# Kernel tuning notes

Measured on AMD Instinct MI355X. Metric: run time of the kernel, lower is better.

## Reference

```python
import jax, jax.numpy as jnp
import numpy as np

B, H, S_PAST, S_NEW, D = 4, 32, 4096, 16, 128


def setup_inputs() -> dict:
    key = jax.random.key(0)
    k1, k2, k3, k4 = jax.random.split(key, 4)
    return {
        "past_key": jax.random.normal(k1, (B, H, S_PAST, D), dtype=jnp.float32),
        "past_value": jax.random.normal(k2, (B, H, S_PAST, D), dtype=jnp.float32),
        "key_states": jax.random.normal(k3, (B, H, S_NEW, D), dtype=jnp.float32),
        "value_states": jax.random.normal(k4, (B, H, S_NEW, D), dtype=jnp.float32),
    }


def reference(past_key, past_value, key_states, value_states):
    # DynamicCache.update: append new tokens along the sequence axis (dim=-2)
    k = jnp.concatenate([past_key, key_states], axis=-2)   # [B,H,S_past+S_new,D]
    v = jnp.concatenate([past_value, value_states], axis=-2)
    return (k, v)
```

## Files before the change

kernel.cpp:

```cpp
#include <hip/hip_runtime.h>


constexpr unsigned B = 4, H = 32, S_PAST = 4096, S_NEW = 16, D = 128;
constexpr unsigned S_TOT = S_PAST + S_NEW;
constexpr unsigned ROW4  = D / 4;
constexpr unsigned CHUNK4 = S_TOT * ROW4;
constexpr unsigned HALF4 = B * H * CHUNK4;
constexpr unsigned TOTAL4 = 2u * HALF4;

__global__ __launch_bounds__(256) void dyncache_concat_kernel(
    const float4* __restrict__ pk, const float4* __restrict__ pv,
    const float4* __restrict__ nk, const float4* __restrict__ nv,
    float4* __restrict__ out)
{
    const unsigned stride = gridDim.x * blockDim.x;
    for (unsigned i = blockIdx.x * blockDim.x + threadIdx.x; i < TOTAL4; i += stride) {
        unsigned j = i;
        const float4* past = pk;
        const float4* neu  = nk;
        if (j >= HALF4) { j -= HALF4; past = pv; neu = nv; }
        const unsigned bh  = j / CHUNK4;
        const unsigned rem = j - bh * CHUNK4;
        const unsigned s   = rem / ROW4;
        const unsigned d4  = rem - s * ROW4;
        float4 val;
        if (s < S_PAST) {
            val = past[(bh * S_PAST + s) * ROW4 + d4];
        } else {
            val = neu[(bh * S_NEW + (s - S_PAST)) * ROW4 + d4];
        }
        out[i] = val;
    }
}

extern "C" void kernel_launch(void* const* d_in, const int* in_sizes, int n_in,
                              void* d_out, int out_size, void* d_ws, size_t ws_size,
                              hipStream_t stream) {
    const float4* pk = (const float4*)d_in[0];
    const float4* pv = (const float4*)d_in[1];
    const float4* nk = (const float4*)d_in[2];
    const float4* nv = (const float4*)d_in[3];
    float4* out = (float4*)d_out;

    dyncache_concat_kernel<<<2048, 256, 0, stream>>>(pk, pv, nk, nv, out);
}
```

Before: 235.4 us.

## Split concat into contiguous block-per-segment copies with nontemporal loads and stores

Replaces the grid-stride loop, which needed per-element division to locate each source row, with a block layout. Each block copies one contiguous segment of the past cache using shift-based addressing, and separate blocks handle the small new-token tails. Loads and stores use nontemporal hints so the streaming data does not pollute the caches. This relies on the shapes being powers of two, which the hardcoded shifts assume.

```diff
diff --git a/kernel.cpp b/kernel.cpp
--- a/kernel.cpp
+++ b/kernel.cpp
@@ -1,46 +1,65 @@
 #include <hip/hip_runtime.h>
 
 
+typedef float f4 __attribute__((ext_vector_type(4)));
+
 constexpr unsigned B = 4, H = 32, S_PAST = 4096, S_NEW = 16, D = 128;
-constexpr unsigned S_TOT = S_PAST + S_NEW;
-constexpr unsigned ROW4  = D / 4;
+constexpr unsigned ROW4   = D / 4;
+constexpr unsigned S_TOT  = S_PAST + S_NEW;
 constexpr unsigned CHUNK4 = S_TOT * ROW4;
-constexpr unsigned HALF4 = B * H * CHUNK4;
-constexpr unsigned TOTAL4 = 2u * HALF4;
+constexpr unsigned HALF4  = B * H * CHUNK4;
+constexpr unsigned PASTC4 = S_PAST * ROW4;
+constexpr unsigned NEWC4  = S_NEW * ROW4;
+constexpr unsigned PAST_TOTAL4 = 2u * B * H * PASTC4;
+constexpr unsigned PAST_BLOCKS = 2048;
+constexpr unsigned SEG4 = PAST_TOTAL4 / PAST_BLOCKS;
+constexpr unsigned NEW_BLOCKS = 2u * B * H;
 
-__global__ __launch_bounds__(256) void dyncache_concat_kernel(
-    const float4* __restrict__ pk, const float4* __restrict__ pv,
-    const float4* __restrict__ nk, const float4* __restrict__ nv,
-    float4* __restrict__ out)
+__global__ __launch_bounds__(256) void dyncache_copy_kernel(
+    const f4* __restrict__ pk, const f4* __restrict__ pv,
+    const f4* __restrict__ nk, const f4* __restrict__ nv,
+    f4* __restrict__ out)
 {
-    const unsigned stride = gridDim.x * blockDim.x;
-    for (unsigned i = blockIdx.x * blockDim.x + threadIdx.x; i < TOTAL4; i += stride) {
-        unsigned j = i;
-        const float4* past = pk;
-        const float4* neu  = nk;
-        if (j >= HALF4) { j -= HALF4; past = pv; neu = nv; }
-        const unsigned bh  = j / CHUNK4;
-        const unsigned rem = j - bh * CHUNK4;
-        const unsigned s   = rem / ROW4;
-        const unsigned d4  = rem - s * ROW4;
-        float4 val;
-        if (s < S_PAST) {
-            val = past[(bh * S_PAST + s) * ROW4 + d4];
-        } else {
-            val = neu[(bh * S_NEW + (s - S_PAST)) * ROW4 + d4];
+    const unsigned tid = threadIdx.x;
+    if (blockIdx.x < PAST_BLOCKS) {
+        const unsigned seg = blockIdx.x * SEG4;
+        const unsigned t   = seg >> 24;
+        const unsigned loc = seg & ((1u << 24) - 1);
+        const unsigned bh  = loc >> 17;
+        const unsigned off = loc & (PASTC4 - 1);
+        const f4* __restrict__ src =
+            (t ? pv : pk) + ((size_t)bh << 17) + off;
+        f4* __restrict__ dst =
+            out + (size_t)t * HALF4 + (size_t)bh * CHUNK4 + off;
+        #pragma unroll 8
+        for (unsigned k = 0; k < SEG4 / 256u; ++k) {
+            const unsigned i = k * 256u + tid;
+            __builtin_nontemporal_store(__builtin_nontemporal_load(src + i), dst + i);
         }
-        out[i] = val;
+    } else {
+        const unsigned blk = blockIdx.x - PAST_BLOCKS;
+        const unsigned t   = blk >> 7;
+        const unsigned bh  = blk & (B * H - 1);
+        const f4* __restrict__ src = (t ? nv : nk) + (size_t)bh * NEWC4;
+        f4* __restrict__ dst =
+            out + (size_t)t * HALF4 + (size_t)bh * CHUNK4 + PASTC4;
+        #pragma unroll
+        for (unsigned k = 0; k < NEWC4 / 256u; ++k) {
+            const unsigned i = k * 256u + tid;
+            __builtin_nontemporal_store(__builtin_nontemporal_load(src + i), dst + i);
+        }
     }
 }
 
 extern "C" void kernel_launch(void* const* d_in, const int* in_sizes, int n_in,
                               void* d_out, int out_size, void* d_ws, size_t ws_size,
                               hipStream_t stream) {
-    const float4* pk = (const float4*)d_in[0];
-    const float4* pv = (const float4*)d_in[1];
-    const float4* nk = (const float4*)d_in[2];
-    const float4* nv = (const float4*)d_in[3];
-    float4* out = (float4*)d_out;
+    const f4* pk = (const f4*)d_in[0];
+    const f4* pv = (const f4*)d_in[1];
+    const f4* nk = (const f4*)d_in[2];
+    const f4* nv = (const f4*)d_in[3];
+    f4* out = (f4*)d_out;
 
-    dyncache_concat_kernel<<<2048, 256, 0, stream>>>(pk, pv, nk, nv, out);
+    dyncache_copy_kernel<<<PAST_BLOCKS + NEW_BLOCKS, 256, 0, stream>>>(
+        pk, pv, nk, nv, out);
 }
```

Measured after the change: 211.3 us. -10.2%, faster.
